# Kernel tuning notes

Hardware: AMD Instinct MI355X
Metric: run time of the kernel (lower is better)

Reference implementation:

```python
import jax, jax.numpy as jnp
import numpy as np
import math

B, CIN, H, W = 32, 128, 64, 64
COUT, KH, KW = 256, 3, 3


def setup_inputs() -> dict:
    key = jax.random.key(0)
    k1, k2, k3 = jax.random.split(key, 3)
    sqrtk = math.sqrt(1.0 / (CIN * KH * KW))
    x = jax.random.normal(k1, (B, CIN, H, W), dtype=jnp.float32)
    weight = jax.random.uniform(k2, (COUT, CIN, KH, KW), dtype=jnp.float32, minval=-sqrtk, maxval=sqrtk)
    bias = jax.random.uniform(k3, (COUT,), dtype=jnp.float32, minval=-sqrtk, maxval=sqrtk)
    return {"input": x, "weight": weight, "bias": bias}


def reference(input, weight, bias):
    # VALID (no padding), stride-1 cross-correlation conv, NCHW/OIHW layout,
    # matching the original nested-loop direct convolution + per-channel bias.
    out = jax.lax.conv_general_dilated(
        input, weight,
        window_strides=(1, 1), padding='VALID',
        dimension_numbers=('NCHW', 'OIHW', 'NCHW'))
    return out + bias[None, :, None, None]
```

## Files before the change

### kernel.cpp

```cpp
#include <hip/hip_runtime.h>

#define NB   32
#define NCI  128
#define NH   64
#define NW   64
#define NCO  256
#define NOH  62
#define NOW  62

typedef __attribute__((ext_vector_type(8))) short bf16x8;
typedef __attribute__((ext_vector_type(8))) unsigned short u16x8;
typedef __attribute__((ext_vector_type(4))) float f32x4;

typedef __attribute__((address_space(1))) const unsigned int glb_u32_t;
typedef __attribute__((address_space(3))) unsigned int lds_u32_t;

__device__ __forceinline__ unsigned short f2bf(float f) {
  unsigned int u = __float_as_uint(f);
  u = u + 0x7FFFu + ((u >> 16) & 1u);
  return (unsigned short)(u >> 16);
}

__device__ __forceinline__ void gload_lds16(const unsigned short* g, unsigned short* l) {
  __builtin_amdgcn_global_load_lds((glb_u32_t*)g, (lds_u32_t*)l, 16, 0, 0);
}

__global__ __launch_bounds__(256) void cvt_x_kernel(const float* __restrict__ x,
                                                    unsigned short* __restrict__ xt) {
  __shared__ unsigned short l[64 * 130];
  const int tid = threadIdx.x;
  const int b = blockIdx.x >> 6, h = blockIdx.x & 63;
  const int w0 = tid & 63, c0 = tid >> 6;
  const float* src = x + ((size_t)b * NCI * NH + h) * NW;
  #pragma unroll
  for (int g = 0; g < 32; ++g) {
    int ci = g * 4 + c0;
    l[w0 * 130 + ci] = f2bf(src[(size_t)ci * (NH * NW) + w0]);
  }
  __syncthreads();
  unsigned short* dst = xt + ((size_t)b * NH + h) * NW * NCI;
  #pragma unroll
  for (int it = 0; it < 4; ++it) {
    int gidx = it * 2048 + tid * 8;
    int w = gidx >> 7, ci0 = gidx & 127;
    const unsigned int* lw = (const unsigned int*)(l + w * 130 + ci0);
    union { u16x8 v; unsigned int u[4]; } t;
    t.u[0] = lw[0]; t.u[1] = lw[1]; t.u[2] = lw[2]; t.u[3] = lw[3];
    *(u16x8*)(dst + w * NCI + ci0) = t.v;
  }
}

__global__ __launch_bounds__(256) void cvt_w_kernel(const float* __restrict__ wsrc,
                                                    unsigned short* __restrict__ wt) {
  int t = blockIdx.x * 256 + threadIdx.x;
  int oc = t & 15, co = (t >> 4) & 255, k = t >> 12;
  const float* src = wsrc + ((size_t)co * NCI + oc * 8) * 9 + k;
  u16x8 v;
  #pragma unroll
  for (int j = 0; j < 8; ++j) v[j] = f2bf(src[j * 9]);
  *(u16x8*)(wt + ((size_t)k * NCO + co) * NCI + oc * 8) = v;
}

__global__ __launch_bounds__(256, 2) void conv_mfma_kernel(
    const unsigned short* __restrict__ xt, const unsigned short* __restrict__ wt,
    const float* __restrict__ bias, float* __restrict__ out) {
  __shared__ unsigned short smem[40960];

  const int tid  = threadIdx.x;
  const int lane = tid & 63;
  const int wid  = tid >> 6;
  const int wn   = wid;
  const int l15  = lane & 15;
  const int lo   = lane >> 4;

  const int bid0  = blockIdx.x;
  const int bid   = (bid0 & 7) * 128 + (bid0 >> 3);
  const int coutg = bid & 1;
  const int ohg   = (bid >> 1) & 15;
  const int b     = bid >> 5;
  const int cbase = coutg * 128;
  const int oh0   = ohg * 4;

  f32x4 acc[8][4];
  #pragma unroll
  for (int mi = 0; mi < 8; ++mi)
    #pragma unroll
    for (int ni = 0; ni < 4; ++ni)
      acc[mi][ni] = (f32x4){0.f, 0.f, 0.f, 0.f};

  const char* sm = (const char*)smem;
  const int af_lane = l15 * 64 + ((lo ^ ((l15 >> 1) & 3)) << 4);

  const size_t xbase = (size_t)b * NH * NW * NCI;
  const unsigned short* xsrc[6];
  #pragma unroll
  for (int i = 0; i < 6; ++i) {
    int e = (wid * 6 + i) * 64 + lane;
    int o = e & 3, w = (e >> 2) & 63, r = e >> 8;
    int row = oh0 + r; if (row > 63) row = 63;
    xsrc[i] = xt + xbase + ((size_t)row * NW + w) * NCI
            + ((o ^ ((w >> 1) & 3)) * 8);
  }
  const unsigned short* wsrc2[2];
  #pragma unroll
  for (int i = 0; i < 2; ++i) {
    int e = (wid * 2 + i) * 64 + lane;
    int o = e & 3, co = e >> 2;
    wsrc2[i] = wt + (size_t)(cbase + co) * NCI + ((o ^ ((co >> 1) & 3)) * 8);
  }

  auto stage_w = [&](int bufq, int t9, int c) {
    unsigned short* dst = smem + 24576 + bufq * 4096;
    const size_t so = (size_t)t9 * NCO * NCI + c * 32;
    #pragma unroll
    for (int i = 0; i < 2; ++i)
      gload_lds16(wsrc2[i] + so, dst + ((wid * 2 + i) * 64 + lane) * 8);
  };
  auto stage_x = [&](int c) {
    unsigned short* dst = smem + (c & 1) * 12288;
    #pragma unroll
    for (int i = 0; i < 6; ++i)
      gload_lds16(xsrc[i] + c * 32, dst + ((wid * 6 + i) * 64 + lane) * 8);
  };

  auto tap_compute = [&](int bufq, int t9, int c) {
    const int kh = t9 / 3, kw = t9 % 3;
    const int r  = wn + kh;
    const int w9 = l15 + kw;
    const int bfl = w9 * 64 + ((lo ^ ((w9 >> 1) & 3)) << 4);
    const char* wsp = sm + 49152 + bufq * 8192;
    const char* xsp = sm + (c & 1) * 24576 + r * 4096;
    bf16x8 af[8], bfv[4];
    #pragma unroll
    for (int mi = 0; mi < 8; ++mi)
      af[mi] = *(const bf16x8*)(wsp + mi * 1024 + af_lane);
    #pragma unroll
    for (int ni = 0; ni < 4; ++ni)
      bfv[ni] = *(const bf16x8*)(xsp + ni * 1024 + bfl);
    __builtin_amdgcn_s_setprio(1);
    #pragma unroll
    for (int mi = 0; mi < 8; ++mi)
      #pragma unroll
      for (int ni = 0; ni < 4; ++ni)
        acc[mi][ni] = __builtin_amdgcn_mfma_f32_16x16x32_bf16(
            af[mi], bfv[ni], acc[mi][ni], 0, 0, 0);
    __builtin_amdgcn_s_setprio(0);
  };

  stage_w(0, 0, 0);
  stage_w(1, 1, 0);
  stage_x(0);

  for (int h = 0; h < 9; ++h) {
    #pragma unroll
    for (int jp = 0; jp < 2; ++jp) {
      const int ta  = h * 4 + jp * 2;
      const int tb  = ta + 1;
      const int t9a = ta % 9, ca = ta / 9;
      const int t9b = tb % 9, cb = tb / 9;
      const int qa  = jp * 2, qb = jp * 2 + 1;
      const int qa2 = (jp * 2 + 2) & 3, qb2 = (jp * 2 + 3) & 3;

      asm volatile("s_waitcnt vmcnt(0)" ::: "memory");
      __builtin_amdgcn_s_barrier();
      __builtin_amdgcn_sched_barrier(0);

      tap_compute(qa, t9a, ca);

      if (ta + 2 <= 35) stage_w(qa2, (ta + 2) % 9, (ta + 2) / 9);
      if (tb + 2 <= 35) stage_w(qb2, (tb + 2) % 9, (tb + 2) / 9);
      if (t9a == 4 && ca < 3) stage_x(ca + 1);
      if (t9b == 4 && cb < 3) stage_x(cb + 1);

      tap_compute(qb, t9b, cb);
    }
  }

  const int oh = oh0 + wn;
  if (oh < NOH) {
    #pragma unroll
    for (int mi = 0; mi < 8; ++mi) {
      int co0 = cbase + mi * 16 + lo * 4;
      const f32x4 bv = *(const f32x4*)(bias + co0);
      #pragma unroll
      for (int ni = 0; ni < 4; ++ni) {
        int ow = ni * 16 + l15;
        if (ow < NOW) {
          size_t o0 = (((size_t)b * NCO + co0) * NOH + oh) * NOW + ow;
          const size_t cs = (size_t)NOH * NOW;
          out[o0]          = acc[mi][ni][0] + bv[0];
          out[o0 + cs]     = acc[mi][ni][1] + bv[1];
          out[o0 + 2 * cs] = acc[mi][ni][2] + bv[2];
          out[o0 + 3 * cs] = acc[mi][ni][3] + bv[3];
        }
      }
    }
  }
}

__global__ __launch_bounds__(256) void conv_naive_kernel(
    const float* __restrict__ x, const float* __restrict__ w,
    const float* __restrict__ bias, float* __restrict__ out) {
  long t = (long)blockIdx.x * 256 + threadIdx.x;
  const long total = (long)NB * NCO * NOH * NOW;
  if (t >= total) return;
  int ow = (int)(t % NOW);
  int oh = (int)((t / NOW) % NOH);
  int co = (int)((t / ((long)NOW * NOH)) % NCO);
  int b  = (int)(t / ((long)NOW * NOH * NCO));
  float acc = bias[co];
  for (int ci = 0; ci < NCI; ++ci) {
    const float* xp = x + (((size_t)b * NCI + ci) * NH + oh) * NW + ow;
    const float* wp = w + ((size_t)co * NCI + ci) * 9;
    #pragma unroll
    for (int kh = 0; kh < 3; ++kh)
      #pragma unroll
      for (int kw = 0; kw < 3; ++kw)
        acc += xp[kh * NW + kw] * wp[kh * 3 + kw];
  }
  out[t] = acc;
}

extern "C" void kernel_launch(void* const* d_in, const int* in_sizes, int n_in,
                              void* d_out, int out_size, void* d_ws, size_t ws_size,
                              hipStream_t stream) {
  const float* x    = (const float*)d_in[0];
  const float* w    = (const float*)d_in[1];
  const float* bias = (const float*)d_in[2];
  float* out        = (float*)d_out;

  const size_t WT_BYTES = (size_t)9 * NCO * NCI * 2;
  const size_t XT_BYTES = (size_t)NB * NH * NW * NCI * 2;

  if (ws_size >= WT_BYTES + XT_BYTES) {
    unsigned short* wt = (unsigned short*)d_ws;
    unsigned short* xt = (unsigned short*)((char*)d_ws + WT_BYTES);
    cvt_w_kernel<<<(9 * NCO * 16) / 256, 256, 0, stream>>>(w, wt);
    cvt_x_kernel<<<NB * NH, 256, 0, stream>>>(x, xt);
    conv_mfma_kernel<<<2 * 16 * NB, 256, 0, stream>>>(xt, wt, bias, out);
  } else {
    const long total = (long)NB * NCO * NOH * NOW;
    conv_naive_kernel<<<(int)((total + 255) / 256), 256, 0, stream>>>(x, w, bias, out);
  }
}
```

Baseline: 101.0 us.

## Restructure conv main loop into per-tap pipeline with partial vmcnt waits

Replaces the two-taps-per-barrier loop, which waited for all outstanding loads (vmcnt(0)), with a single per-tap loop. Each tap issues its LDS fragment reads, issues the global-to-LDS prefetch for tap t+2 (and the next x chunk), then waits with a partial vmcnt count so loads stay in flight across the barrier. The intent is to overlap global loads with MFMA work more continuously and to stop draining the memory queue at every barrier. In exchange there is one barrier per tap instead of per pair, and correctness now depends on hand-counted vmcnt values matching the number of outstanding loads.

After: 97.85 us. -3.2%, faster.

```diff
diff --git a/kernel.cpp b/kernel.cpp
--- a/kernel.cpp
+++ b/kernel.cpp
@@ -109,9 +109,9 @@
     wsrc2[i] = wt + (size_t)(cbase + co) * NCI + ((o ^ ((co >> 1) & 3)) * 8);
   }
 
-  auto stage_w = [&](int bufq, int t9, int c) {
-    unsigned short* dst = smem + 24576 + bufq * 4096;
-    const size_t so = (size_t)t9 * NCO * NCI + c * 32;
+  auto stage_w = [&](int t) {
+    unsigned short* dst = smem + 24576 + (t & 3) * 4096;
+    const size_t so = (size_t)(t % 9) * NCO * NCI + (t / 9) * 32;
     #pragma unroll
     for (int i = 0; i < 2; ++i)
       gload_lds16(wsrc2[i] + so, dst + ((wid * 2 + i) * 64 + lane) * 8);
@@ -123,13 +123,21 @@
       gload_lds16(xsrc[i] + c * 32, dst + ((wid * 6 + i) * 64 + lane) * 8);
   };
 
-  auto tap_compute = [&](int bufq, int t9, int c) {
-    const int kh = t9 / 3, kw = t9 % 3;
-    const int r  = wn + kh;
-    const int w9 = l15 + kw;
+  stage_w(0);
+  stage_w(1);
+  stage_x(0);
+  asm volatile("s_waitcnt vmcnt(0)" ::: "memory");
+  __builtin_amdgcn_s_barrier();
+  __builtin_amdgcn_sched_barrier(0);
+
+  for (int t = 0; t < 36; ++t) {
+    const int t9 = t % 9, c = t / 9;
+    const int kh = t9 / 3, kw = t9 - kh * 3;
+
+    const char* wsp = sm + 49152 + (t & 3) * 8192;
+    const char* xsp = sm + (c & 1) * 24576 + (wn + kh) * 4096;
+    const int w9  = l15 + kw;
     const int bfl = w9 * 64 + ((lo ^ ((w9 >> 1) & 3)) << 4);
-    const char* wsp = sm + 49152 + bufq * 8192;
-    const char* xsp = sm + (c & 1) * 24576 + r * 4096;
     bf16x8 af[8], bfv[4];
     #pragma unroll
     for (int mi = 0; mi < 8; ++mi)
@@ -137,6 +145,23 @@
     #pragma unroll
     for (int ni = 0; ni < 4; ++ni)
       bfv[ni] = *(const bf16x8*)(xsp + ni * 1024 + bfl);
+
+    if (t + 2 < 36) stage_w(t + 2);
+    const bool xstage = (t9 == 3) && (c < 3);
+    if (xstage) stage_x(c + 1);
+
+    __builtin_amdgcn_sched_barrier(0);
+    if (t >= 34) {
+      asm volatile("s_waitcnt vmcnt(0)" ::: "memory");
+    } else if (xstage || (t9 == 4 && c < 3)) {
+      asm volatile("s_waitcnt vmcnt(8)" ::: "memory");
+    } else {
+      asm volatile("s_waitcnt vmcnt(2)" ::: "memory");
+    }
+    __builtin_amdgcn_s_barrier();
+    asm volatile("s_waitcnt lgkmcnt(0)" ::: "memory");
+    __builtin_amdgcn_sched_barrier(0);
+
     __builtin_amdgcn_s_setprio(1);
     #pragma unroll
     for (int mi = 0; mi < 8; ++mi)
@@ -145,35 +170,6 @@
         acc[mi][ni] = __builtin_amdgcn_mfma_f32_16x16x32_bf16(
             af[mi], bfv[ni], acc[mi][ni], 0, 0, 0);
     __builtin_amdgcn_s_setprio(0);
-  };
-
-  stage_w(0, 0, 0);
-  stage_w(1, 1, 0);
-  stage_x(0);
-
-  for (int h = 0; h < 9; ++h) {
-    #pragma unroll
-    for (int jp = 0; jp < 2; ++jp) {
-      const int ta  = h * 4 + jp * 2;
-      const int tb  = ta + 1;
-      const int t9a = ta % 9, ca = ta / 9;
-      const int t9b = tb % 9, cb = tb / 9;
-      const int qa  = jp * 2, qb = jp * 2 + 1;
-      const int qa2 = (jp * 2 + 2) & 3, qb2 = (jp * 2 + 3) & 3;
-
-      asm volatile("s_waitcnt vmcnt(0)" ::: "memory");
-      __builtin_amdgcn_s_barrier();
-      __builtin_amdgcn_sched_barrier(0);
-
-      tap_compute(qa, t9a, ca);
-
-      if (ta + 2 <= 35) stage_w(qa2, (ta + 2) % 9, (ta + 2) / 9);
-      if (tb + 2 <= 35) stage_w(qb2, (tb + 2) % 9, (tb + 2) / 9);
-      if (t9a == 4 && ca < 3) stage_x(ca + 1);
-      if (t9b == 4 && cb < 3) stage_x(cb + 1);
-
-      tap_compute(qb, t9b, cb);
-    }
   }
 
   const int oh = oh0 + wn;
```
